# Kernel optimization log

Measured on AMD Instinct MI355X. Metric: run time of the kernel, lower is better.

## Reference

```python
import jax, jax.numpy as jnp
import numpy as np

DIM = 4096
N_HEADS = 32
N_KV_HEADS = 8
HEAD_DIM = 128
WINDOW = 1024
SEQ = 2048
ROPE_THETA = 10000.0


def setup_inputs() -> dict:
    key = jax.random.key(0)
    ks = jax.random.split(key, 5)
    x = jax.random.normal(ks[0], (SEQ, DIM), dtype=jnp.float32)
    # torch nn.Linear weights are [out_features, in_features]
    wq = jax.random.normal(ks[1], (N_HEADS * HEAD_DIM, DIM), dtype=jnp.float32) * (DIM ** -0.5)
    wk = jax.random.normal(ks[2], (N_KV_HEADS * HEAD_DIM, DIM), dtype=jnp.float32) * (DIM ** -0.5)
    wv = jax.random.normal(ks[3], (N_KV_HEADS * HEAD_DIM, DIM), dtype=jnp.float32) * (DIM ** -0.5)
    wo = jax.random.normal(ks[4], (DIM, N_HEADS * HEAD_DIM), dtype=jnp.float32) * ((N_HEADS * HEAD_DIM) ** -0.5)
    # RoPE freqs: freqs_cis[t, i] = exp(1j * t * theta^(-2i/d)); store cos/sin
    inv_freq = ROPE_THETA ** (-jnp.arange(0, HEAD_DIM, 2, dtype=jnp.float32) / HEAD_DIM)  # [D/2]
    angles = jnp.arange(SEQ, dtype=jnp.float32)[:, None] * inv_freq[None, :]  # [S, D/2]
    return {"x": x, "wq": wq, "wk": wk, "wv": wv, "wo": wo,
            "cos": jnp.cos(angles), "sin": jnp.sin(angles)}


def _apply_rope(t, cos, sin):
    # t: [S, H, D]; cos/sin: [S, D/2] -> rotate consecutive pairs as complex mul
    S, H, D = t.shape
    tr = t.reshape(S, H, D // 2, 2)
    t0, t1 = tr[..., 0], tr[..., 1]
    c = cos[:, None, :]
    s = sin[:, None, :]
    out = jnp.stack([t0 * c - t1 * s, t0 * s + t1 * c], axis=-1)
    return out.reshape(S, H, D)


def reference(x, wq, wk, wv, wo, cos, sin):
    S = x.shape[0]
    repeats = N_HEADS // N_KV_HEADS
    scale = HEAD_DIM ** -0.5
    q = (x @ wq.T).reshape(S, N_HEADS, HEAD_DIM)
    k = (x @ wk.T).reshape(S, N_KV_HEADS, HEAD_DIM)
    v = (x @ wv.T).reshape(S, N_KV_HEADS, HEAD_DIM)
    q = _apply_rope(q, cos, sin)
    k = _apply_rope(k, cos, sin)
    # repeat_kv: repeat_interleave along head axis (GQA)
    k = jnp.repeat(k, repeats, axis=1)  # [S, H, D]
    v = jnp.repeat(v, repeats, axis=1)
    scores = jnp.einsum('qhd,khd->hqk', q, k) * scale  # [H, S, S]
    # sliding-window causal mask: attend to j in (i - WINDOW, i]
    i = jnp.arange(S)[:, None]
    j = jnp.arange(S)[None, :]
    allowed = (j <= i) & (i - j < WINDOW)  # [S, S]
    scores = jnp.where(allowed[None, :, :], scores, jnp.finfo(scores.dtype).min)
    probs = jax.nn.softmax(scores, axis=-1)
    out = jnp.einsum('hqk,khd->qhd', probs, v).reshape(S, N_HEADS * HEAD_DIM)
    return out @ wo.T
```

## Files before the change

kernel.cpp:

```cpp
#include <hip/hip_runtime.h>

#define DIM 4096
#define NH 32
#define NKV 8
#define HD 128
#define WINDOW 1024
#define SEQ 2048
#define QLD 6144

typedef unsigned int uint32;
typedef __attribute__((ext_vector_type(8))) short short8_t;
typedef __attribute__((ext_vector_type(8))) __bf16 bf16x8_t;
typedef __attribute__((ext_vector_type(4))) float floatx4_t;

__device__ __forceinline__ uint32 f2bf_bits(float f) {
  uint32 u = __builtin_bit_cast(uint32, f);
  return (u + 0x7fffu + ((u >> 16) & 1u)) >> 16;
}
__device__ __forceinline__ float bf2f(unsigned short b) {
  return __builtin_bit_cast(float, ((uint32)b) << 16);
}

template <class X, class Y> struct same_t { static constexpr bool v = false; };
template <class X> struct same_t<X, X> { static constexpr bool v = true; };

__device__ __forceinline__ void load_lds16(const unsigned short* g, unsigned short* l) {
  __builtin_amdgcn_global_load_lds((__attribute__((address_space(1))) void*)g,
                                   (__attribute__((address_space(3))) void*)l, 16, 0, 0);
}

template <typename TC, bool ROPE, int JT>
__global__ __launch_bounds__(256, 2) void gemm_bf16(const unsigned short* __restrict__ A,
                                                    const unsigned short* __restrict__ B,
                                                    TC* __restrict__ C,
                                                    int M, int N, int K,
                                                    const float* __restrict__ cosp,
                                                    const float* __restrict__ sinp,
                                                    int rope_ncols) {
  constexpr int BN = 32 * JT;
  constexpr int WN = 16 * JT;
  __shared__ unsigned short As[128 * 64];
  __shared__ unsigned short Bs[BN * 64];
  const int tid = threadIdx.x;
  const int lane = tid & 63, w = tid >> 6;
  const int quad = lane >> 4, l16 = lane & 15;
  const int wm = w >> 1, wn = w & 1;
  const size_t m0 = (size_t)blockIdx.y * 128, n0 = (size_t)blockIdx.x * BN;

  const int srow = tid >> 3;
  const int scol = ((tid & 7) ^ (srow & 7)) << 3;
  const unsigned short* Abase = A + (m0 + srow) * (size_t)K + scol;
  const unsigned short* Bbase = B + (n0 + srow) * (size_t)K + scol;
  unsigned short* ldsA = As + (tid >> 6) * 512;
  unsigned short* ldsB = Bs + (tid >> 6) * 512;

  const int sa = l16 & 7;
  const int raA = wm * 64 + l16;
  const int raB = wn * WN + l16;

  floatx4_t acc[4][JT] = {};

  const int nk = K >> 6;
  for (int kt = 0; kt < nk; kt++) {
    const int kbase = kt << 6;
#pragma unroll
    for (int i = 0; i < 4; i++)
      load_lds16(Abase + kbase + (size_t)(i * 32) * K, ldsA + i * 2048);
#pragma unroll
    for (int i = 0; i < JT; i++)
      load_lds16(Bbase + kbase + (size_t)(i * 32) * K, ldsB + i * 2048);
    __syncthreads();
#pragma unroll
    for (int ks = 0; ks < 2; ks++) {
      bf16x8_t af[4], bfg[JT];
#pragma unroll
      for (int i = 0; i < 4; i++) {
        const int colA = (((ks << 2) | quad) ^ sa) << 3;
        af[i] = __builtin_bit_cast(bf16x8_t,
            *(const short8_t*)(&As[(raA + i * 16) * 64 + colA]));
      }
#pragma unroll
      for (int j = 0; j < JT; j++) {
        const int colB = (((ks << 2) | quad) ^ sa) << 3;
        bfg[j] = __builtin_bit_cast(bf16x8_t,
            *(const short8_t*)(&Bs[(raB + j * 16) * 64 + colB]));
      }
#pragma unroll
      for (int i = 0; i < 4; i++)
#pragma unroll
        for (int j = 0; j < JT; j++)
          acc[i][j] = __builtin_amdgcn_mfma_f32_16x16x32_bf16(af[i], bfg[j], acc[i][j], 0, 0, 0);
    }
    __syncthreads();
  }
#pragma unroll
  for (int i = 0; i < 4; i++)
#pragma unroll
    for (int j = 0; j < JT; j++) {
      const int colb = (int)n0 + wn * WN + j * 16;
      const bool do_rope = ROPE && (colb < rope_ncols);
#pragma unroll
      for (int r = 0; r < 4; r++) {
        size_t row = m0 + wm * 64 + i * 16 + quad * 4 + r;
        size_t col = n0 + wn * WN + j * 16 + l16;
        float v = acc[i][j][r];
        if constexpr (ROPE) {
          if (do_rope) {
            float pv = __shfl_xor(v, 1);
            const int d = ((int)col & 127) >> 1;
            const float c = cosp[row * 64 + d];
            const float s = sinp[row * 64 + d];
            v = ((int)col & 1) ? (pv * s + v * c) : (v * c - pv * s);
          }
        }
        if constexpr (same_t<TC, float>::v)
          C[row * (size_t)N + col] = v;
        else
          C[row * (size_t)N + col] = (unsigned short)f2bf_bits(v);
      }
    }
}

__global__ __launch_bounds__(256) void cvt_kernel(const float* __restrict__ in,
                                                  unsigned short* __restrict__ out, int n8) {
  int idx = blockIdx.x * 256 + threadIdx.x;
  if (idx >= n8) return;
  const float4* p = (const float4*)in + (size_t)idx * 2;
  float4 a = p[0], b = p[1];
  uint32 w0 = f2bf_bits(a.x) | (f2bf_bits(a.y) << 16);
  uint32 w1 = f2bf_bits(a.z) | (f2bf_bits(a.w) << 16);
  uint32 w2 = f2bf_bits(b.x) | (f2bf_bits(b.y) << 16);
  uint32 w3 = f2bf_bits(b.z) | (f2bf_bits(b.w) << 16);
  ((uint4*)out)[idx] = make_uint4(w0, w1, w2, w3);
}

__global__ __launch_bounds__(256) void cvt4_kernel(const float* __restrict__ s0,
                                                   const float* __restrict__ s1,
                                                   const float* __restrict__ s2,
                                                   const float* __restrict__ s3,
                                                   unsigned short* __restrict__ d0,
                                                   unsigned short* __restrict__ d1,
                                                   unsigned short* __restrict__ d2,
                                                   unsigned short* __restrict__ d3) {
  const int b = blockIdx.x;
  const float* src;
  unsigned short* dst;
  int rb;
  if (b < 4096)        { src = s0; dst = d0; rb = b; }
  else if (b < 12288)  { src = s1; dst = d1; rb = b - 4096; }
  else if (b < 14336)  { src = s2; dst = d2; rb = b - 12288; }
  else                 { src = s3; dst = d3; rb = b - 14336; }
  const int idx = rb * 256 + threadIdx.x;
  const float4* p = (const float4*)src + (size_t)idx * 2;
  float4 a = p[0], bb = p[1];
  uint32 w0 = f2bf_bits(a.x) | (f2bf_bits(a.y) << 16);
  uint32 w1 = f2bf_bits(a.z) | (f2bf_bits(a.w) << 16);
  uint32 w2 = f2bf_bits(bb.x) | (f2bf_bits(bb.y) << 16);
  uint32 w3 = f2bf_bits(bb.z) | (f2bf_bits(bb.w) << 16);
  ((uint4*)dst)[idx] = make_uint4(w0, w1, w2, w3);
}

__global__ __launch_bounds__(256) void vtrans_kernel(const unsigned short* __restrict__ v,
                                                     unsigned short* __restrict__ vT) {
  __shared__ unsigned short t[64][72];
  const int s0 = blockIdx.y * 64, r0 = blockIdx.x * 64;
  const int tid = threadIdx.x;
#pragma unroll
  for (int it = 0; it < 2; it++) {
    int f = it * 256 + tid;
    int si = f >> 3, cj = (f & 7) << 3;
    *(short8_t*)(&t[si][cj]) = *(const short8_t*)(v + (size_t)(s0 + si) * QLD + r0 + cj);
  }
  __syncthreads();
#pragma unroll
  for (int it = 0; it < 2; it++) {
    int f = it * 256 + tid;
    int ri = f >> 3, sj = (f & 7) << 3;
    short8_t o;
#pragma unroll
    for (int jj = 0; jj < 8; jj++) o[jj] = t[sj + jj][ri];
    *(short8_t*)(vT + (size_t)(r0 + ri) * SEQ + s0 + sj) = o;
  }
}

__global__ __launch_bounds__(256, 3) void attn_kernel(const unsigned short* __restrict__ qb,
                                                      const unsigned short* __restrict__ kb,
                                                      const unsigned short* __restrict__ vT,
                                                      unsigned short* __restrict__ attn_out) {
  const int h = blockIdx.x;
  const int qt = 31 - blockIdx.y;
  const int kvh = h >> 2;
  const int q0 = qt * 64;
  const int tid = threadIdx.x;
  const int w = tid >> 6, lane = tid & 63;
  const int quad = lane >> 4, l16 = lane & 15;
  const float SCALE = 0.08838834764831845f;

  __shared__ unsigned short Ks[64 * 128];
  __shared__ unsigned short VTs[128 * 64];
  __shared__ unsigned short PTs[4 * 64 * 34];

  unsigned short* pt = &PTs[w * 2176];

  const int krow = tid >> 4;
  const int kc16 = tid & 15;
  const int kgcol = (kc16 ^ (krow & 7)) << 3;
  const unsigned short* kgbase = kb + (size_t)krow * QLD + kvh * 128 + kgcol;
  const int vrow = tid >> 3;
  const int vc8 = tid & 7;
  const int vgcol = (vc8 ^ (vrow & 7)) << 3;
  const unsigned short* vgbase = vT + (size_t)(kvh * 128 + vrow) * 2048 + vgcol;
  unsigned short* ldsK = Ks + w * 512;
  unsigned short* ldsV = VTs + w * 512;

  bf16x8_t aq[4];
  {
    const unsigned short* qp = qb + (size_t)(q0 + w * 16 + l16) * QLD + h * 128 + quad * 8;
#pragma unroll
    for (int ks = 0; ks < 4; ks++)
      aq[ks] = __builtin_bit_cast(bf16x8_t, *(const short8_t*)(qp + ks * 32));
  }

  floatx4_t O[8] = {};
  float m_run[4], l_run[4];
#pragma unroll
  for (int r = 0; r < 4; r++) { m_run[r] = -3e38f; l_run[r] = 0.0f; }

  const int qmin = q0 + w * 16, qmax = qmin + 15;
  int kbeg = q0 - (WINDOW - 1); if (kbeg < 0) kbeg = 0;
  const int c0 = kbeg & ~63;
  const int nch = (q0 + 64 - c0) >> 6;
  const int sa = l16 & 7;

  for (int ci = 0; ci < nch; ci++) {
    const int kb0 = c0 + (ci << 6);
#pragma unroll
    for (int i = 0; i < 4; i++)
      load_lds16(kgbase + (size_t)(kb0 + i * 16) * QLD, ldsK + i * 2048);
#pragma unroll
    for (int i = 0; i < 4; i++)
      load_lds16(vgbase + kb0 + (size_t)(i * 32) * 2048, ldsV + i * 2048);
    __syncthreads();
    floatx4_t S[4];
#pragma unroll
    for (int j = 0; j < 4; j++) {
      floatx4_t acc = {};
      const int keyrow = j * 16 + l16;
#pragma unroll
      for (int ks = 0; ks < 4; ks++) {
        const int c16 = ((ks << 2) | quad) ^ sa;
        bf16x8_t bfk = __builtin_bit_cast(bf16x8_t,
            *(const short8_t*)(&Ks[keyrow * 128 + c16 * 8]));
        acc = __builtin_amdgcn_mfma_f32_16x16x32_bf16(aq[ks], bfk, acc, 0, 0, 0);
      }
      S[j] = acc;
    }
    const bool need_mask = (kb0 + 63 > qmin) || (qmax - kb0 >= WINDOW);
    if (need_mask) {
#pragma unroll
      for (int j = 0; j < 4; j++) {
        const int key = kb0 + j * 16 + l16;
#pragma unroll
        for (int r = 0; r < 4; r++) {
          const int i = qmin + quad * 4 + r;
          const bool ok = (key <= i) && (i - key < WINDOW);
          S[j][r] = ok ? S[j][r] : -3e38f;
        }
      }
    }
    float mx[4], rs[4], alpha[4];
#pragma unroll
    for (int r = 0; r < 4; r++) {
      float m = S[0][r];
#pragma unroll
      for (int j = 1; j < 4; j++) m = fmaxf(m, S[j][r]);
#pragma unroll
      for (int d = 1; d < 16; d <<= 1) m = fmaxf(m, __shfl_xor(m, d, 16));
      mx[r] = fmaxf(m_run[r], m);
      alpha[r] = __expf(SCALE * (m_run[r] - mx[r]));
      m_run[r] = mx[r];
      rs[r] = 0.0f;
    }
#pragma unroll
    for (int j = 0; j < 4; j++) {
      float p[4];
#pragma unroll
      for (int r = 0; r < 4; r++) {
        const float sv = S[j][r];
        float e = __expf(SCALE * (sv - mx[r]));
        if (need_mask) e = (sv < -1e37f) ? 0.0f : e;
        p[r] = e;
        rs[r] += e;
      }
      uint32* dst = (uint32*)(pt + (j * 16 + l16) * 34 + quad * 4);
      dst[0] = f2bf_bits(p[0]) | (f2bf_bits(p[1]) << 16);
      dst[1] = f2bf_bits(p[2]) | (f2bf_bits(p[3]) << 16);
    }
#pragma unroll
    for (int r = 0; r < 4; r++) {
#pragma unroll
      for (int d = 1; d < 16; d <<= 1) rs[r] += __shfl_xor(rs[r], d, 16);
      l_run[r] = l_run[r] * alpha[r] + rs[r];
    }
#pragma unroll
    for (int nt = 0; nt < 8; nt++)
#pragma unroll
      for (int r = 0; r < 4; r++) O[nt][r] *= alpha[r];
    asm volatile("" ::: "memory");
#pragma unroll
    for (int ks = 0; ks < 2; ks++) {
      short8_t as;
#pragma unroll
      for (int jj = 0; jj < 8; jj++)
        as[jj] = (short)pt[(ks * 32 + quad * 8 + jj) * 34 + l16];
      bf16x8_t af = __builtin_bit_cast(bf16x8_t, as);
#pragma unroll
      for (int nt = 0; nt < 8; nt++) {
        const int c8 = (((ks << 2) | quad) ^ sa);
        bf16x8_t bfv = __builtin_bit_cast(bf16x8_t,
            *(const short8_t*)(&VTs[(nt * 16 + l16) * 64 + c8 * 8]));
        O[nt] = __builtin_amdgcn_mfma_f32_16x16x32_bf16(af, bfv, O[nt], 0, 0, 0);
      }
    }
    __syncthreads();
  }
  float inv_l[4];
#pragma unroll
  for (int r = 0; r < 4; r++) inv_l[r] = 1.0f / l_run[r];
#pragma unroll
  for (int nt = 0; nt < 8; nt++)
#pragma unroll
    for (int r = 0; r < 4; r++) {
      float v = O[nt][r] * inv_l[r];
      attn_out[(size_t)(qmin + quad * 4 + r) * 4096 + h * 128 + nt * 16 + l16] =
          (unsigned short)f2bf_bits(v);
    }
}

extern "C" void kernel_launch(void* const* d_in, const int* in_sizes, int n_in,
                              void* d_out, int out_size, void* d_ws, size_t ws_size,
                              hipStream_t stream) {
  (void)in_sizes; (void)n_in; (void)out_size; (void)ws_size;
  const float* x    = (const float*)d_in[0];
  const float* wq   = (const float*)d_in[1];
  const float* wk   = (const float*)d_in[2];
  const float* wv   = (const float*)d_in[3];
  const float* wo   = (const float*)d_in[4];
  const float* cosp = (const float*)d_in[5];
  const float* sinp = (const float*)d_in[6];
  float* out = (float*)d_out;
  char* ws = (char*)d_ws;

  unsigned short* wqkvb = (unsigned short*)(ws);
  unsigned short* wob   = (unsigned short*)(ws);
  unsigned short* vTb   = (unsigned short*)(ws + 33554432);
  unsigned short* xb    = (unsigned short*)(ws + 50331648);
  unsigned short* attnb = (unsigned short*)(ws + 50331648);
  unsigned short* qkvb  = (unsigned short*)(ws + 67108864);

  cvt4_kernel<<<16384, 256, 0, stream>>>(
      x, wq, wk, wv,
      xb, wqkvb, wqkvb + (size_t)4096 * 4096, wqkvb + (size_t)5120 * 4096);
  gemm_bf16<unsigned short, true, 6><<<dim3(32, 16), 256, 0, stream>>>(
      xb, wqkvb, qkvb, SEQ, QLD, DIM, cosp, sinp, 5120);
  cvt_kernel<<<8192, 256, 0, stream>>>(wo, wob, DIM * NH * HD / 8);
  vtrans_kernel<<<dim3(16, 32), 256, 0, stream>>>(qkvb + 5120, vTb);
  attn_kernel<<<dim3(NH, 32), 256, 0, stream>>>(qkvb, qkvb + 4096, vTb, attnb);
  gemm_bf16<float, false, 4><<<dim3(32, 16), 256, 0, stream>>>(
      attnb, wob, out, SEQ, 4096, DIM, nullptr, nullptr, 0);
}
```

Baseline: 467.9 us.

## Enlarge attention query tile to 128 rows, fuse wo-convert with V transpose

The attention kernel now uses 512-thread blocks covering 128 query rows, so each K/V chunk staged in shared memory serves eight waves instead of four. Waves whose rows fall entirely outside a chunk's causal or window range skip that chunk's compute. The P staging layout is changed so the PV operand is read as one vector load, and s_setprio raises wave priority around the MFMA sections. The wo conversion and V transpose are merged into one launch to save a kernel launch. The cost is half as many blocks and more idle waves at the diagonal and window edges.

After: 465.0 us. No clear change (-0.6%).

```diff
diff --git a/kernel.cpp b/kernel.cpp
--- a/kernel.cpp
+++ b/kernel.cpp
@@ -119,19 +119,6 @@
           C[row * (size_t)N + col] = (unsigned short)f2bf_bits(v);
       }
     }
-}
-
-__global__ __launch_bounds__(256) void cvt_kernel(const float* __restrict__ in,
-                                                  unsigned short* __restrict__ out, int n8) {
-  int idx = blockIdx.x * 256 + threadIdx.x;
-  if (idx >= n8) return;
-  const float4* p = (const float4*)in + (size_t)idx * 2;
-  float4 a = p[0], b = p[1];
-  uint32 w0 = f2bf_bits(a.x) | (f2bf_bits(a.y) << 16);
-  uint32 w1 = f2bf_bits(a.z) | (f2bf_bits(a.w) << 16);
-  uint32 w2 = f2bf_bits(b.x) | (f2bf_bits(b.y) << 16);
-  uint32 w3 = f2bf_bits(b.z) | (f2bf_bits(b.w) << 16);
-  ((uint4*)out)[idx] = make_uint4(w0, w1, w2, w3);
 }
 
 __global__ __launch_bounds__(256) void cvt4_kernel(const float* __restrict__ s0,
@@ -160,11 +147,26 @@
   ((uint4*)dst)[idx] = make_uint4(w0, w1, w2, w3);
 }
 
-__global__ __launch_bounds__(256) void vtrans_kernel(const unsigned short* __restrict__ v,
-                                                     unsigned short* __restrict__ vT) {
+__global__ __launch_bounds__(256) void epi_kernel(const float* __restrict__ wo,
+                                                  unsigned short* __restrict__ wob,
+                                                  const unsigned short* __restrict__ v,
+                                                  unsigned short* __restrict__ vT) {
   __shared__ unsigned short t[64][72];
-  const int s0 = blockIdx.y * 64, r0 = blockIdx.x * 64;
+  const int b = blockIdx.x;
   const int tid = threadIdx.x;
+  if (b < 8192) {
+    const int idx = b * 256 + tid;
+    const float4* p = (const float4*)wo + (size_t)idx * 2;
+    float4 a = p[0], bb = p[1];
+    uint32 w0 = f2bf_bits(a.x) | (f2bf_bits(a.y) << 16);
+    uint32 w1 = f2bf_bits(a.z) | (f2bf_bits(a.w) << 16);
+    uint32 w2 = f2bf_bits(bb.x) | (f2bf_bits(bb.y) << 16);
+    uint32 w3 = f2bf_bits(bb.z) | (f2bf_bits(bb.w) << 16);
+    ((uint4*)wob)[idx] = make_uint4(w0, w1, w2, w3);
+    return;
+  }
+  const int bx = b - 8192;
+  const int r0 = (bx & 15) * 64, s0 = (bx >> 4) * 64;
 #pragma unroll
   for (int it = 0; it < 2; it++) {
     int f = it * 256 + tid;
@@ -183,14 +185,14 @@
   }
 }
 
-__global__ __launch_bounds__(256, 3) void attn_kernel(const unsigned short* __restrict__ qb,
+__global__ __launch_bounds__(512, 4) void attn_kernel(const unsigned short* __restrict__ qb,
                                                       const unsigned short* __restrict__ kb,
                                                       const unsigned short* __restrict__ vT,
                                                       unsigned short* __restrict__ attn_out) {
   const int h = blockIdx.x;
-  const int qt = 31 - blockIdx.y;
+  const int qt = 15 - blockIdx.y;
   const int kvh = h >> 2;
-  const int q0 = qt * 64;
+  const int q0 = qt * 128;
   const int tid = threadIdx.x;
   const int w = tid >> 6, lane = tid & 63;
   const int quad = lane >> 4, l16 = lane & 15;
@@ -198,9 +200,9 @@
 
   __shared__ unsigned short Ks[64 * 128];
   __shared__ unsigned short VTs[128 * 64];
-  __shared__ unsigned short PTs[4 * 64 * 34];
-
-  unsigned short* pt = &PTs[w * 2176];
+  __shared__ unsigned short PTs[8 * 16 * 72];
+
+  unsigned short* pt = &PTs[w * 1152];
 
   const int krow = tid >> 4;
   const int kc16 = tid & 15;
@@ -229,98 +231,102 @@
   const int qmin = q0 + w * 16, qmax = qmin + 15;
   int kbeg = q0 - (WINDOW - 1); if (kbeg < 0) kbeg = 0;
   const int c0 = kbeg & ~63;
-  const int nch = (q0 + 64 - c0) >> 6;
+  const int nch = (q0 + 128 - c0) >> 6;
   const int sa = l16 & 7;
 
   for (int ci = 0; ci < nch; ci++) {
     const int kb0 = c0 + (ci << 6);
 #pragma unroll
-    for (int i = 0; i < 4; i++)
-      load_lds16(kgbase + (size_t)(kb0 + i * 16) * QLD, ldsK + i * 2048);
-#pragma unroll
-    for (int i = 0; i < 4; i++)
-      load_lds16(vgbase + kb0 + (size_t)(i * 32) * 2048, ldsV + i * 2048);
+    for (int i = 0; i < 2; i++)
+      load_lds16(kgbase + (size_t)(kb0 + i * 32) * QLD, ldsK + i * 4096);
+#pragma unroll
+    for (int i = 0; i < 2; i++)
+      load_lds16(vgbase + kb0 + (size_t)(i * 64) * 2048, ldsV + i * 4096);
     __syncthreads();
-    floatx4_t S[4];
-#pragma unroll
-    for (int j = 0; j < 4; j++) {
-      floatx4_t acc = {};
-      const int keyrow = j * 16 + l16;
-#pragma unroll
-      for (int ks = 0; ks < 4; ks++) {
-        const int c16 = ((ks << 2) | quad) ^ sa;
-        bf16x8_t bfk = __builtin_bit_cast(bf16x8_t,
-            *(const short8_t*)(&Ks[keyrow * 128 + c16 * 8]));
-        acc = __builtin_amdgcn_mfma_f32_16x16x32_bf16(aq[ks], bfk, acc, 0, 0, 0);
-      }
-      S[j] = acc;
-    }
-    const bool need_mask = (kb0 + 63 > qmin) || (qmax - kb0 >= WINDOW);
-    if (need_mask) {
+    const bool alive = (kb0 <= qmax) && (kb0 + 63 >= qmin - (WINDOW - 1));
+    if (alive) {
+      floatx4_t S[4];
+      __builtin_amdgcn_s_setprio(1);
 #pragma unroll
       for (int j = 0; j < 4; j++) {
-        const int key = kb0 + j * 16 + l16;
+        floatx4_t acc = {};
+        const int keyrow = j * 16 + l16;
+#pragma unroll
+        for (int ks = 0; ks < 4; ks++) {
+          const int c16 = ((ks << 2) | quad) ^ sa;
+          bf16x8_t bfk = __builtin_bit_cast(bf16x8_t,
+              *(const short8_t*)(&Ks[keyrow * 128 + c16 * 8]));
+          acc = __builtin_amdgcn_mfma_f32_16x16x32_bf16(aq[ks], bfk, acc, 0, 0, 0);
+        }
+        S[j] = acc;
+      }
+      __builtin_amdgcn_s_setprio(0);
+      const bool need_mask = (kb0 + 63 > qmin) || (qmax - kb0 >= WINDOW);
+      if (need_mask) {
+#pragma unroll
+        for (int j = 0; j < 4; j++) {
+          const int key = kb0 + j * 16 + l16;
+#pragma unroll
+          for (int r = 0; r < 4; r++) {
+            const int i = qmin + quad * 4 + r;
+            const bool ok = (key <= i) && (i - key < WINDOW);
+            S[j][r] = ok ? S[j][r] : -3e38f;
+          }
+        }
+      }
+      float mx[4], rs[4], alpha[4];
+#pragma unroll
+      for (int r = 0; r < 4; r++) {
+        float m = S[0][r];
+#pragma unroll
+        for (int j = 1; j < 4; j++) m = fmaxf(m, S[j][r]);
+#pragma unroll
+        for (int d = 1; d < 16; d <<= 1) m = fmaxf(m, __shfl_xor(m, d, 16));
+        mx[r] = fmaxf(m_run[r], m);
+        alpha[r] = __expf(SCALE * (m_run[r] - mx[r]));
+        m_run[r] = mx[r];
+        rs[r] = 0.0f;
+      }
+#pragma unroll
+      for (int j = 0; j < 4; j++) {
+        float p[4];
 #pragma unroll
         for (int r = 0; r < 4; r++) {
-          const int i = qmin + quad * 4 + r;
-          const bool ok = (key <= i) && (i - key < WINDOW);
-          S[j][r] = ok ? S[j][r] : -3e38f;
-        }
-      }
-    }
-    float mx[4], rs[4], alpha[4];
-#pragma unroll
-    for (int r = 0; r < 4; r++) {
-      float m = S[0][r];
-#pragma unroll
-      for (int j = 1; j < 4; j++) m = fmaxf(m, S[j][r]);
-#pragma unroll
-      for (int d = 1; d < 16; d <<= 1) m = fmaxf(m, __shfl_xor(m, d, 16));
-      mx[r] = fmaxf(m_run[r], m);
-      alpha[r] = __expf(SCALE * (m_run[r] - mx[r]));
-      m_run[r] = mx[r];
-      rs[r] = 0.0f;
-    }
-#pragma unroll
-    for (int j = 0; j < 4; j++) {
-      float p[4];
+          const float sv = S[j][r];
+          float e = __expf(SCALE * (sv - mx[r]));
+          if (need_mask) e = (sv < -1e37f) ? 0.0f : e;
+          p[r] = e;
+          rs[r] += e;
+        }
+#pragma unroll
+        for (int r = 0; r < 4; r++)
+          pt[(quad * 4 + r) * 72 + j * 16 + l16] = (unsigned short)f2bf_bits(p[r]);
+      }
 #pragma unroll
       for (int r = 0; r < 4; r++) {
-        const float sv = S[j][r];
-        float e = __expf(SCALE * (sv - mx[r]));
-        if (need_mask) e = (sv < -1e37f) ? 0.0f : e;
-        p[r] = e;
-        rs[r] += e;
-      }
-      uint32* dst = (uint32*)(pt + (j * 16 + l16) * 34 + quad * 4);
-      dst[0] = f2bf_bits(p[0]) | (f2bf_bits(p[1]) << 16);
-      dst[1] = f2bf_bits(p[2]) | (f2bf_bits(p[3]) << 16);
-    }
-#pragma unroll
-    for (int r = 0; r < 4; r++) {
-#pragma unroll
-      for (int d = 1; d < 16; d <<= 1) rs[r] += __shfl_xor(rs[r], d, 16);
-      l_run[r] = l_run[r] * alpha[r] + rs[r];
-    }
-#pragma unroll
-    for (int nt = 0; nt < 8; nt++)
-#pragma unroll
-      for (int r = 0; r < 4; r++) O[nt][r] *= alpha[r];
-    asm volatile("" ::: "memory");
-#pragma unroll
-    for (int ks = 0; ks < 2; ks++) {
-      short8_t as;
-#pragma unroll
-      for (int jj = 0; jj < 8; jj++)
-        as[jj] = (short)pt[(ks * 32 + quad * 8 + jj) * 34 + l16];
-      bf16x8_t af = __builtin_bit_cast(bf16x8_t, as);
-#pragma unroll
-      for (int nt = 0; nt < 8; nt++) {
-        const int c8 = (((ks << 2) | quad) ^ sa);
-        bf16x8_t bfv = __builtin_bit_cast(bf16x8_t,
-            *(const short8_t*)(&VTs[(nt * 16 + l16) * 64 + c8 * 8]));
-        O[nt] = __builtin_amdgcn_mfma_f32_16x16x32_bf16(af, bfv, O[nt], 0, 0, 0);
-      }
+#pragma unroll
+        for (int d = 1; d < 16; d <<= 1) rs[r] += __shfl_xor(rs[r], d, 16);
+        l_run[r] = l_run[r] * alpha[r] + rs[r];
+      }
+#pragma unroll
+      for (int nt = 0; nt < 8; nt++)
+#pragma unroll
+        for (int r = 0; r < 4; r++) O[nt][r] *= alpha[r];
+      asm volatile("" ::: "memory");
+      __builtin_amdgcn_s_setprio(1);
+#pragma unroll
+      for (int ks = 0; ks < 2; ks++) {
+        bf16x8_t af = __builtin_bit_cast(bf16x8_t,
+            *(const short8_t*)(&pt[l16 * 72 + ks * 32 + quad * 8]));
+#pragma unroll
+        for (int nt = 0; nt < 8; nt++) {
+          const int c8 = (((ks << 2) | quad) ^ sa);
+          bf16x8_t bfv = __builtin_bit_cast(bf16x8_t,
+              *(const short8_t*)(&VTs[(nt * 16 + l16) * 64 + c8 * 8]));
+          O[nt] = __builtin_amdgcn_mfma_f32_16x16x32_bf16(af, bfv, O[nt], 0, 0, 0);
+        }
+      }
+      __builtin_amdgcn_s_setprio(0);
     }
     __syncthreads();
   }
@@ -363,9 +369,8 @@
       xb, wqkvb, wqkvb + (size_t)4096 * 4096, wqkvb + (size_t)5120 * 4096);
   gemm_bf16<unsigned short, true, 6><<<dim3(32, 16), 256, 0, stream>>>(
       xb, wqkvb, qkvb, SEQ, QLD, DIM, cosp, sinp, 5120);
-  cvt_kernel<<<8192, 256, 0, stream>>>(wo, wob, DIM * NH * HD / 8);
-  vtrans_kernel<<<dim3(16, 32), 256, 0, stream>>>(qkvb + 5120, vTb);
-  attn_kernel<<<dim3(NH, 32), 256, 0, stream>>>(qkvb, qkvb + 4096, vTb, attnb);
+  epi_kernel<<<8704, 256, 0, stream>>>(wo, wob, qkvb + 5120, vTb);
+  attn_kernel<<<dim3(NH, 16), 512, 0, stream>>>(qkvb, qkvb + 4096, vTb, attnb);
   gemm_bf16<float, false, 4><<<dim3(32, 16), 256, 0, stream>>>(
       attnb, wob, out, SEQ, 4096, DIM, nullptr, nullptr, 0);
 }
```
